# Kernel optimization log

Measured on AMD Instinct MI355X. Metric: run time of the kernel, lower is better.

Reference implementation:

```python
import jax, jax.numpy as jnp
import numpy as np

N, E, IN = 50000, 800000, 64
HC, FC1, FC2, FC3, OUT = 96, 256, 128, 64, 8
EPS = 1e-5


def setup_inputs() -> dict:
    key = jax.random.key(0)
    ks = jax.random.split(key, 24)
    def lin(k, fi, fo):
        # kaiming_uniform with relu gain: bound = sqrt(6/fi)
        b = np.sqrt(6.0 / fi)
        return jax.random.uniform(k, (fi, fo), jnp.float32, -b, b)
    inp = {
        'x': jax.random.normal(ks[0], (N, IN), jnp.float32),
        'edge_index': jax.random.randint(ks[1], (2, E), 0, N, jnp.int64),
        'w1': lin(ks[2], IN, HC), 'b1': jnp.zeros((HC,), jnp.float32),
        'g1': jax.random.uniform(ks[3], (HC,), jnp.float32, 0.5, 1.5), 'be1': jax.random.normal(ks[4], (HC,), jnp.float32) * 0.1,
        'w2': lin(ks[5], HC, HC), 'b2': jnp.zeros((HC,), jnp.float32),
        'g2': jax.random.uniform(ks[6], (HC,), jnp.float32, 0.5, 1.5), 'be2': jax.random.normal(ks[7], (HC,), jnp.float32) * 0.1,
        'w3': lin(ks[8], HC, HC), 'b3': jnp.zeros((HC,), jnp.float32),
        'g3': jax.random.uniform(ks[9], (HC,), jnp.float32, 0.5, 1.5), 'be3': jax.random.normal(ks[10], (HC,), jnp.float32) * 0.1,
        'lw1': lin(ks[11], HC, FC1), 'lb1': jnp.zeros((FC1,), jnp.float32),
        'lw2': lin(ks[12], FC1, FC2), 'lb2': jnp.zeros((FC2,), jnp.float32),
        'lw3': lin(ks[13], FC2, FC3), 'lb3': jnp.zeros((FC3,), jnp.float32),
        'lw4': lin(ks[14], FC3, OUT), 'lb4': jnp.zeros((OUT,), jnp.float32),
    }
    return inp


def _gcn(x, w, b, src, dst, norm):
    # GCNConv: out[dst] += norm_e * (x @ w)[src]; then + bias
    h = x @ w
    msg = h[src] * norm[:, None]
    return jax.ops.segment_sum(msg, dst, num_segments=N) + b


def _bn_eval(x, g, be):
    # eval-mode BatchNorm1d with running_mean=0, running_var=1
    return x / jnp.sqrt(1.0 + EPS) * g + be


def reference(x, edge_index, w1, b1, g1, be1, w2, b2, g2, be2, w3, b3, g3, be3,
              lw1, lb1, lw2, lb2, lw3, lb3, lw4, lb4):
    loops = jnp.arange(N, dtype=edge_index.dtype)
    src = jnp.concatenate([edge_index[0], loops])
    dst = jnp.concatenate([edge_index[1], loops])
    deg = jax.ops.segment_sum(jnp.ones_like(src, jnp.float32), dst, num_segments=N)
    dinv = jax.lax.rsqrt(deg)  # deg >= 1 due to self loops
    norm = dinv[src] * dinv[dst]

    h = jax.nn.relu(_bn_eval(_gcn(x, w1, b1, src, dst, norm), g1, be1))
    h = jax.nn.relu(_bn_eval(_gcn(h, w2, b2, src, dst, norm), g2, be2))
    h = jax.nn.relu(_bn_eval(_gcn(h, w3, b3, src, dst, norm), g3, be3))
    h = jax.nn.relu(h @ lw1 + lb1)
    h = jax.nn.relu(h @ lw2 + lb2)
    h = jax.nn.relu(h @ lw3 + lb3)
    return h @ lw4 + lb4
```

## Files before the change

### kernel.cpp

```cpp
#include <hip/hip_runtime.h>


#define GN 50000
#define GE 800000
#define NPART 98
#define PSLOT 9216
#define CHK 2048

typedef __attribute__((ext_vector_type(8))) short bf16x8;
typedef __attribute__((ext_vector_type(4))) float floatx4;

__device__ __forceinline__ float ar1_b2f(unsigned short h) {
    return __uint_as_float(((unsigned)h) << 16);
}
__device__ __forceinline__ unsigned short ar1_f2b(float f) {
    unsigned u = __float_as_uint(f);
    u = u + 0x7FFFu + ((u >> 16) & 1u);
    return (unsigned short)(u >> 16);
}

__global__ void ar1_detect(const int* ei, const unsigned short* xw,
                           int* flagI, int* flagF, int* gcur) {
    __shared__ int cnt;
    if (threadIdx.x == 0) cnt = 0;
    __syncthreads();
    if (blockIdx.x == 0) {
        if ((int)threadIdx.x < NPART) gcur[threadIdx.x] = 0;
        if (ei[2 * threadIdx.x + 1] != 0) atomicAdd(&cnt, 1);
        __syncthreads();
        if (threadIdx.x == 0) flagI[0] = (cnt < 8) ? 1 : 0;
    } else {
        unsigned short w = xw[2 * threadIdx.x];
        int ex = (w >> 7) & 0xFF;
        if (w == 0 || (ex >= 90 && ex <= 150)) atomicAdd(&cnt, 1);
        __syncthreads();
        if (threadIdx.x == 0) flagF[0] = (cnt > 200) ? 0 : 1;
    }
}

__global__ __launch_bounds__(256)
void ar1_part(const int* __restrict__ ei, const int* __restrict__ flagI,
              int* __restrict__ gcur, unsigned int* __restrict__ pairs, int E) {
    __shared__ int cnt[NPART], base[NPART], cur[NPART];
    int tid = (int)threadIdx.x;
    for (int i = tid; i < NPART; i += 256) { cnt[i] = 0; cur[i] = 0; }
    __syncthreads();
    int is64 = flagI[0];
    int e0 = (int)blockIdx.x * CHK;
    unsigned pk[8]; int q[8];
#pragma unroll
    for (int k = 0; k < 8; k++) {
        int e = e0 + k * 256 + tid;
        q[k] = -1; pk[k] = 0;
        if (e < E) {
            int s = is64 ? ei[2 * e] : ei[e];
            int d = is64 ? ei[2 * (E + e)] : ei[E + e];
            if ((unsigned)s < (unsigned)GN && (unsigned)d < (unsigned)GN) {
                int qq = d >> 9;
                q[k] = qq;
                pk[k] = (unsigned)s | ((unsigned)(d & 511) << 17);
                atomicAdd(&cnt[qq], 1);
            }
        }
    }
    __syncthreads();
    for (int i = tid; i < NPART; i += 256)
        base[i] = (cnt[i] > 0) ? atomicAdd(&gcur[i], cnt[i]) : 0;
    __syncthreads();
#pragma unroll
    for (int k = 0; k < 8; k++) {
        if (q[k] >= 0) {
            int r = base[q[k]] + atomicAdd(&cur[q[k]], 1);
            if (r < PSLOT) pairs[(size_t)q[k] * PSLOT + r] = pk[k];
        }
    }
}

__global__ void ar1_pscan(const int* gcur, int* pbase) {
    __shared__ int sm[128];
    int tid = (int)threadIdx.x;
    int v = (tid < NPART) ? gcur[tid] : 0;
    sm[tid] = v;
    __syncthreads();
    for (int off = 1; off < 128; off <<= 1) {
        int t = (tid >= off) ? sm[tid - off] : 0;
        __syncthreads();
        sm[tid] += t;
        __syncthreads();
    }
    if (tid < NPART) pbase[tid] = sm[tid] - v;
}

__global__ __launch_bounds__(256)
void ar1_csr(const unsigned int* __restrict__ pairs, const int* __restrict__ gcur,
             const int* __restrict__ pbase, int* __restrict__ csr,
             int* __restrict__ indeg, int* __restrict__ offs,
             float* __restrict__ dinv) {
    __shared__ int ncnt[512], pre[512], cur[512], psum[16];
    int p = (int)blockIdx.x, tid = (int)threadIdx.x;
    int cntE = gcur[p];
    if (cntE > PSLOT) cntE = PSLOT;
    int gbase = pbase[p];
    for (int i = tid; i < 512; i += 256) ncnt[i] = 0;
    __syncthreads();
    const unsigned int* pp = pairs + (size_t)p * PSLOT;
    for (int i = tid; i < cntE; i += 256) atomicAdd(&ncnt[pp[i] >> 17], 1);
    __syncthreads();
    if (tid < 16) {
        int s = 0;
        for (int j = tid * 32; j < tid * 32 + 32; j++) { pre[j] = s; s += ncnt[j]; }
        psum[tid] = s;
    }
    __syncthreads();
    if (tid == 0) {
        int s = 0;
        for (int j = 0; j < 16; j++) { int t = psum[j]; psum[j] = s; s += t; }
    }
    __syncthreads();
    if (tid < 16)
        for (int j = tid * 32; j < tid * 32 + 32; j++) pre[j] += psum[tid];
    __syncthreads();
    for (int j = tid; j < 512; j += 256) {
        cur[j] = pre[j];
        int node = p * 512 + j;
        if (node < GN) {
            indeg[node] = ncnt[j];
            offs[node] = gbase + pre[j];
            dinv[node] = rsqrtf((float)(ncnt[j] + 1));
        }
    }
    __syncthreads();
    for (int i = tid; i < cntE; i += 256) {
        unsigned v = pp[i];
        int r = atomicAdd(&cur[v >> 17], 1);
        csr[gbase + r] = (int)(v & 0x1FFFFu);
    }
}

struct SmallCvt {
    const void* src[4];
    float* dst[4];
    int n[4];
    const void* gb[9];
    float* ss[6];
};
__global__ void ar1_cvt_small(SmallCvt sc, const int* flagF) {
    int f = flagF[0];
    const float C = 0.9999950000374997f;
    for (int s = 0; s < 4; s++) {
        for (int i = threadIdx.x; i < sc.n[s]; i += 256) {
            float v = f ? ((const float*)sc.src[s])[i]
                        : ar1_b2f(((const unsigned short*)sc.src[s])[i]);
            sc.dst[s][i] = v;
        }
    }
    for (int k = 0; k < 3; k++) {
        for (int i = threadIdx.x; i < 96; i += 256) {
            float b, g, be;
            if (f) {
                b  = ((const float*)sc.gb[3 * k + 0])[i];
                g  = ((const float*)sc.gb[3 * k + 1])[i];
                be = ((const float*)sc.gb[3 * k + 2])[i];
            } else {
                b  = ar1_b2f(((const unsigned short*)sc.gb[3 * k + 0])[i]);
                g  = ar1_b2f(((const unsigned short*)sc.gb[3 * k + 1])[i]);
                be = ar1_b2f(((const unsigned short*)sc.gb[3 * k + 2])[i]);
            }
            sc.ss[2 * k + 0][i] = C * g;
            sc.ss[2 * k + 1][i] = b * C * g + be;
        }
    }
}

struct PackAll {
    const void* src[7];
    unsigned short* dst[7];
    int K[7], M[7], start[8];
};
__global__ void ar1_pack_all(PackAll pa, const int* flagF) {
    int b = (int)blockIdx.x;
    int w = 0;
    while (w < 6 && b >= pa.start[w + 1]) w++;
    int frag = b - pa.start[w];
    int K = pa.K[w], M = pa.M[w];
    int lane = (int)threadIdx.x;
    int nch = K >> 5;
    int t = frag / nch, c = frag - t * nch;
    int n = t * 16 + (lane & 15);
    int k0 = c * 32 + (lane >> 4) * 8;
    int f = flagF[0];
    unsigned short* o = pa.dst[w] + ((size_t)frag * 64 + lane) * 8;
    for (int j = 0; j < 8; j++) {
        unsigned short v = 0;
        if (n < M) {
            int idx = (k0 + j) * M + n;
            v = f ? ar1_f2b(((const float*)pa.src[w])[idx])
                  : ((const unsigned short*)pa.src[w])[idx];
        }
        o[j] = v;
    }
}

template <int NT>
__global__ __launch_bounds__(256, 2)
void ar1_mfma(const unsigned short* __restrict__ A,
              const unsigned short* __restrict__ Bp,
              const float* __restrict__ scale, const float* __restrict__ shift,
              unsigned short* __restrict__ C, int K, int Astride, int Cstride,
              int Mout) {
    int tid = (int)threadIdx.x;
    int wv = tid >> 6, lane = tid & 63;
    int mb = ((int)blockIdx.x * 4 + wv) * 16;
    int m = lane & 15, quad = lane >> 4;
    int arow = mb + m;
    if (arow >= GN) arow = GN - 1;
    const unsigned short* Aptr = A + (size_t)arow * Astride + quad * 8;
    int nch = K >> 5;

    floatx4 acc[NT];
#pragma unroll
    for (int t = 0; t < NT; t++) acc[t] = (floatx4){0.f, 0.f, 0.f, 0.f};

    for (int c = 0; c < nch; c++) {
        bf16x8 a = *((const bf16x8*)(Aptr + c * 32));
#pragma unroll
        for (int t = 0; t < NT; t++) {
            bf16x8 b = *((const bf16x8*)(Bp + ((size_t)(t * nch + c) * 64 + lane) * 8));
            acc[t] = __builtin_amdgcn_mfma_f32_16x16x32_bf16(a, b, acc[t], 0, 0, 0);
        }
    }

#pragma unroll
    for (int t = 0; t < NT; t++) {
#pragma unroll
        for (int r = 0; r < 4; r++) {
            int row = mb + quad * 4 + r;
            int col = t * 16 + m;
            if (row < GN && col < Mout) {
                float v = acc[t][r] * scale[col] + shift[col];
                C[(size_t)row * Cstride + col] = ar1_f2b(fmaxf(v, 0.f));
            }
        }
    }
}

__global__ __launch_bounds__(256, 2)
void ar1_mlp(const unsigned short* __restrict__ A,
             const unsigned short* __restrict__ b3,
             const unsigned short* __restrict__ b4,
             const unsigned short* __restrict__ b5,
             const unsigned short* __restrict__ b6,
             const float* __restrict__ lb0, const float* __restrict__ lb1,
             const float* __restrict__ lb2, const float* __restrict__ lb3,
             void* __restrict__ out, const int* __restrict__ f32out) {
    __shared__ unsigned short H1[64 * 264];
    __shared__ unsigned short H2[64 * 136];
    __shared__ unsigned short H3[64 * 72];
    int tid = (int)threadIdx.x, wv = tid >> 6, lane = tid & 63;
    int m = lane & 15, quad = lane >> 4;
    int mb = (int)blockIdx.x * 64 + wv * 16;
    int lwv = wv * 16;

    {
        int arow = mb + m; if (arow >= GN) arow = GN - 1;
        const unsigned short* Ap = A + (size_t)arow * 128 + quad * 8;
        floatx4 acc[16];
#pragma unroll
        for (int t = 0; t < 16; t++) acc[t] = (floatx4){0.f, 0.f, 0.f, 0.f};
        for (int c = 0; c < 3; c++) {
            bf16x8 a = *((const bf16x8*)(Ap + c * 32));
#pragma unroll
            for (int t = 0; t < 16; t++) {
                bf16x8 b = *((const bf16x8*)(b3 + ((size_t)(t * 3 + c) * 64 + lane) * 8));
                acc[t] = __builtin_amdgcn_mfma_f32_16x16x32_bf16(a, b, acc[t], 0, 0, 0);
            }
        }
#pragma unroll
        for (int t = 0; t < 16; t++)
#pragma unroll
            for (int r = 0; r < 4; r++) {
                int lr = lwv + quad * 4 + r, col = t * 16 + m;
                H1[lr * 264 + col] = ar1_f2b(fmaxf(acc[t][r] + lb0[col], 0.f));
            }
    }
    {
        const unsigned short* Hp = H1 + (size_t)(lwv + m) * 264 + quad * 8;
        floatx4 acc[8];
#pragma unroll
        for (int t = 0; t < 8; t++) acc[t] = (floatx4){0.f, 0.f, 0.f, 0.f};
        for (int c = 0; c < 8; c++) {
            bf16x8 a = *((const bf16x8*)(Hp + c * 32));
#pragma unroll
            for (int t = 0; t < 8; t++) {
                bf16x8 b = *((const bf16x8*)(b4 + ((size_t)(t * 8 + c) * 64 + lane) * 8));
                acc[t] = __builtin_amdgcn_mfma_f32_16x16x32_bf16(a, b, acc[t], 0, 0, 0);
            }
        }
#pragma unroll
        for (int t = 0; t < 8; t++)
#pragma unroll
            for (int r = 0; r < 4; r++) {
                int lr = lwv + quad * 4 + r, col = t * 16 + m;
                H2[lr * 136 + col] = ar1_f2b(fmaxf(acc[t][r] + lb1[col], 0.f));
            }
    }
    {
        const unsigned short* Hp = H2 + (size_t)(lwv + m) * 136 + quad * 8;
        floatx4 acc[4];
#pragma unroll
        for (int t = 0; t < 4; t++) acc[t] = (floatx4){0.f, 0.f, 0.f, 0.f};
        for (int c = 0; c < 4; c++) {
            bf16x8 a = *((const bf16x8*)(Hp + c * 32));
#pragma unroll
            for (int t = 0; t < 4; t++) {
                bf16x8 b = *((const bf16x8*)(b5 + ((size_t)(t * 4 + c) * 64 + lane) * 8));
                acc[t] = __builtin_amdgcn_mfma_f32_16x16x32_bf16(a, b, acc[t], 0, 0, 0);
            }
        }
#pragma unroll
        for (int t = 0; t < 4; t++)
#pragma unroll
            for (int r = 0; r < 4; r++) {
                int lr = lwv + quad * 4 + r, col = t * 16 + m;
                H3[lr * 72 + col] = ar1_f2b(fmaxf(acc[t][r] + lb2[col], 0.f));
            }
    }
    {
        const unsigned short* Hp = H3 + (size_t)(lwv + m) * 72 + quad * 8;
        floatx4 acc = (floatx4){0.f, 0.f, 0.f, 0.f};
        for (int c = 0; c < 2; c++) {
            bf16x8 a = *((const bf16x8*)(Hp + c * 32));
            bf16x8 b = *((const bf16x8*)(b6 + ((size_t)c * 64 + lane) * 8));
            acc = __builtin_amdgcn_mfma_f32_16x16x32_bf16(a, b, acc, 0, 0, 0);
        }
        int wf32 = f32out[0];
#pragma unroll
        for (int r = 0; r < 4; r++) {
            int row = mb + quad * 4 + r;
            if (row < GN && m < 8) {
                float v = acc[r] + lb3[m];
                if (wf32) ((float*)out)[(size_t)row * 8 + m] = v;
                else ((unsigned short*)out)[(size_t)row * 8 + m] = ar1_f2b(v);
            }
        }
    }
}

__global__ __launch_bounds__(256, 8)
void ar1_agg64(const unsigned short* __restrict__ X, const int* __restrict__ offs,
               const int* __restrict__ indeg, const int* __restrict__ csr,
               const float* __restrict__ dinv, unsigned short* __restrict__ Out) {
    int wv = (int)threadIdx.x >> 6, lane = (int)threadIdx.x & 63;
    int node = (int)blockIdx.x * 4 + wv;
    if (node >= GN) return;
    int chunk = lane & 7;
    int eslot = lane >> 3;
    float di = dinv[node];
    int off = offs[node], cnt = indeg[node];

    float acc[8];
#pragma unroll
    for (int j = 0; j < 8; j++) acc[j] = 0.f;

    for (int base = 0; base < cnt; base += 16) {
        int ss[2]; float ww[2];
#pragma unroll
        for (int k = 0; k < 2; k++) {
            int e = base + k * 8 + eslot;
            int s = node; float w = 0.f;
            if (e < cnt) {
                s = csr[off + e];
                if ((unsigned)s >= (unsigned)GN) s = node;
                w = dinv[s] * di;
            }
            ss[k] = s; ww[k] = w;
        }
        bf16x8 h0 = *((const bf16x8*)(X + (size_t)ss[0] * 64 + chunk * 8));
        bf16x8 h1 = *((const bf16x8*)(X + (size_t)ss[1] * 64 + chunk * 8));
#pragma unroll
        for (int j = 0; j < 8; j++)
            acc[j] += ww[0] * ar1_b2f((unsigned short)h0[j])
                    + ww[1] * ar1_b2f((unsigned short)h1[j]);
    }

#pragma unroll
    for (int j = 0; j < 8; j++) {
        acc[j] += __shfl_xor(acc[j], 8, 64);
        acc[j] += __shfl_xor(acc[j], 16, 64);
        acc[j] += __shfl_xor(acc[j], 32, 64);
    }

    if (eslot == 0) {
        bf16x8 hs = *((const bf16x8*)(X + (size_t)node * 64 + chunk * 8));
#pragma unroll
        for (int j = 0; j < 8; j++) {
            float v = acc[j] + di * di * ar1_b2f((unsigned short)hs[j]);
            Out[(size_t)node * 64 + chunk * 8 + j] = ar1_f2b(v);
        }
    }
}

__global__ __launch_bounds__(256, 8)
void ar1_agg96(const unsigned short* __restrict__ H, const int* __restrict__ offs,
               const int* __restrict__ indeg, const int* __restrict__ csr,
               const float* __restrict__ dinv, unsigned short* __restrict__ Out) {
    int wv = (int)threadIdx.x >> 6, lane = (int)threadIdx.x & 63;
    int node = (int)blockIdx.x * 4 + wv;
    if (node >= GN) return;
    int chunk = lane & 15;
    int eslot = lane >> 4;
    float di = dinv[node];
    int off = offs[node], cnt = indeg[node];

    float acc[8];
#pragma unroll
    for (int j = 0; j < 8; j++) acc[j] = 0.f;

    for (int base = 0; base < cnt; base += 16) {
        int ss[4]; float ww[4]; bf16x8 hh[4];
#pragma unroll
        for (int k = 0; k < 4; k++) {
            int e = base + k * 4 + eslot;
            int s = node; float w = 0.f;
            if (e < cnt) {
                s = csr[off + e];
                if ((unsigned)s >= (unsigned)GN) s = node;
                w = dinv[s] * di;
            }
            ss[k] = s; ww[k] = w;
        }
#pragma unroll
        for (int k = 0; k < 4; k++)
            hh[k] = *((const bf16x8*)(H + (size_t)ss[k] * 128 + chunk * 8));
#pragma unroll
        for (int k = 0; k < 4; k++)
#pragma unroll
            for (int j = 0; j < 8; j++)
                acc[j] += ww[k] * ar1_b2f((unsigned short)hh[k][j]);
    }

#pragma unroll
    for (int j = 0; j < 8; j++) {
        acc[j] += __shfl_xor(acc[j], 16, 64);
        acc[j] += __shfl_xor(acc[j], 32, 64);
    }

    if (eslot == 0 && chunk < 12) {
        bf16x8 hs = *((const bf16x8*)(H + (size_t)node * 128 + chunk * 8));
#pragma unroll
        for (int j = 0; j < 8; j++) {
            float v = acc[j] + di * di * ar1_b2f((unsigned short)hs[j]);
            Out[(size_t)node * 128 + chunk * 8 + j] = ar1_f2b(v);
        }
    }
}

__global__ void Arthur1_16458314678864_kernel(const void* src,
                                              unsigned short* dst, int n,
                                              const int* flagF) {
    int i = blockIdx.x * 256 + threadIdx.x;
    if (i < n) {
        if (flagF[0]) dst[i] = ar1_f2b(((const float*)src)[i]);
        else          dst[i] = ((const unsigned short*)src)[i];
    }
}

extern "C" void kernel_launch(void* const* d_in, const int* in_sizes, int n_in,
                              void* d_out, int out_size, void* d_ws, size_t ws_size,
                              hipStream_t stream) {
    (void)in_sizes; (void)n_in; (void)out_size;

    char* p = (char*)d_ws;
    unsigned short* bufA = (unsigned short*)p; p += (size_t)GN * 128 * 2;
    unsigned short* bufC = (unsigned short*)p; p += (size_t)GN * 128 * 2;
    unsigned short* bufX = (unsigned short*)p; p += (size_t)GN * 64 * 2;
    unsigned int* pairs = (unsigned int*)p; p += (size_t)NPART * PSLOT * 4;
    int* indeg  = (int*)p;    p += (size_t)GN * 4;
    int* offs   = (int*)p;    p += (size_t)GN * 4;
    float* dinv = (float*)p;  p += (size_t)GN * 4;
    int* csr    = (int*)p;    p += (size_t)GE * 4;
    int* gcur   = (int*)p;    p += 1024;
    int* pbase  = (int*)p;    p += 1024;
    int* flagI  = (int*)p;    p += 1024;
    int* flagF  = (int*)p;    p += 1024;
    unsigned short* bpArena = (unsigned short*)p; p += 91136 * 2;
    float* fArena = (float*)p; p += 2048 * 4;
    size_t need = (size_t)(p - (char*)d_ws);
    if (ws_size < need) {
        hipMemsetAsync(d_out, 0x41, (size_t)GN * 8 * 2, stream);
        return;
    }

    unsigned short* bp[7];
    int bpn[7] = {6144, 9216, 9216, 24576, 32768, 8192, 1024};
    {
        unsigned short* q = bpArena;
        for (int i = 0; i < 7; i++) { bp[i] = q; q += bpn[i]; }
    }

    float* lb[4]; float* ss[6];
    {
        float* q = fArena;
        int ln[4] = {256, 128, 64, 8};
        for (int i = 0; i < 4; i++) { lb[i] = q; q += ln[i]; }
        for (int i = 0; i < 6; i++) { ss[i] = q; q += 96; }
    }

    const int* ei = (const int*)d_in[1];

    ar1_detect<<<2, 256, 0, stream>>>(ei, (const unsigned short*)d_in[0], flagI, flagF, gcur);
    ar1_part<<<(GE + CHK - 1) / CHK, 256, 0, stream>>>(ei, flagI, gcur, pairs, GE);
    ar1_pscan<<<1, 128, 0, stream>>>(gcur, pbase);
    ar1_csr<<<NPART, 256, 0, stream>>>(pairs, gcur, pbase, csr, indeg, offs, dinv);

    Arthur1_16458314678864_kernel<<<(GN * 64 + 255) / 256, 256, 0, stream>>>(
        d_in[0], bufX, GN * 64, flagF);
    {
        SmallCvt sc;
        int lsrc[4] = {15, 17, 19, 21};
        int ln[4] = {256, 128, 64, 8};
        for (int i = 0; i < 4; i++) { sc.src[i] = d_in[lsrc[i]]; sc.dst[i] = lb[i]; sc.n[i] = ln[i]; }
        int gsrc[9] = {3, 4, 5, 7, 8, 9, 11, 12, 13};
        for (int i = 0; i < 9; i++) sc.gb[i] = d_in[gsrc[i]];
        for (int i = 0; i < 6; i++) sc.ss[i] = ss[i];
        ar1_cvt_small<<<1, 256, 0, stream>>>(sc, flagF);
    }
    {
        PackAll pa;
        int wsrc[7] = {2, 6, 10, 14, 16, 18, 20};
        int Ks[7] = {64, 96, 96, 96, 256, 128, 64};
        int Ms[7] = {96, 96, 96, 256, 128, 64, 8};
        int cum = 0;
        for (int i = 0; i < 7; i++) {
            pa.src[i] = d_in[wsrc[i]]; pa.dst[i] = bp[i];
            pa.K[i] = Ks[i]; pa.M[i] = Ms[i];
            pa.start[i] = cum;
            cum += (Ms[i] + 15) / 16 * (Ks[i] / 32);
        }
        pa.start[7] = cum;
        ar1_pack_all<<<cum, 64, 0, stream>>>(pa, flagF);
    }

    const int GB = (GN + 63) / 64;
    const int AB = GN / 4;

    ar1_agg64<<<AB, 256, 0, stream>>>(bufX, offs, indeg, csr, dinv, bufC);
    ar1_mfma<6><<<GB, 256, 0, stream>>>(bufC, bp[0], ss[0], ss[1], bufA, 64, 64, 128, 96);
    ar1_agg96<<<AB, 256, 0, stream>>>(bufA, offs, indeg, csr, dinv, bufC);
    ar1_mfma<6><<<GB, 256, 0, stream>>>(bufC, bp[1], ss[2], ss[3], bufA, 96, 128, 128, 96);
    ar1_agg96<<<AB, 256, 0, stream>>>(bufA, offs, indeg, csr, dinv, bufC);
    ar1_mfma<6><<<GB, 256, 0, stream>>>(bufC, bp[2], ss[4], ss[5], bufA, 96, 128, 128, 96);

    ar1_mlp<<<GB, 256, 0, stream>>>(bufA, bp[3], bp[4], bp[5], bp[6],
                                    lb[0], lb[1], lb[2], lb[3], d_out, flagF);
}
```

Before: 331.5 us.

## Pack hidden buffers to 96-wide rows, read input directly, merge setup kernels

Hidden activation buffers shrink from a 128-element row stride to 96, so the gathers in aggregation and the matmul stores move less padding, and agg96 is re-laned to use 48 of 64 lanes with 12 chunks. The separate kernel that converted x to bf16 is removed; agg64 now reads the raw input in fp32 or bf16 depending on a flag. The small-parameter conversion and weight-packing kernels are fused into one launch to cut launch overhead. The cost is a quarter of the lanes idle in agg96, shuffle-based reductions in place of xor butterflies, and fp32 gathers of x in the first layer.

Result: faster. 324.7 us (-2.0%).

```diff
diff --git a/kernel.cpp b/kernel.cpp
--- a/kernel.cpp
+++ b/kernel.cpp
@@ -137,6 +137,11 @@
     }
 }
 
+struct PackAll {
+    const void* src[7];
+    unsigned short* dst[7];
+    int K[7], M[7], start[8];
+};
 struct SmallCvt {
     const void* src[4];
     float* dst[4];
@@ -144,60 +149,58 @@
     const void* gb[9];
     float* ss[6];
 };
-__global__ void ar1_cvt_small(SmallCvt sc, const int* flagF) {
+
+__global__ void Arthur1_16458314678864_kernel(PackAll pa, SmallCvt sc,
+                                              const int* flagF) {
+    int b = (int)blockIdx.x;
     int f = flagF[0];
-    const float C = 0.9999950000374997f;
-    for (int s = 0; s < 4; s++) {
-        for (int i = threadIdx.x; i < sc.n[s]; i += 256) {
-            float v = f ? ((const float*)sc.src[s])[i]
-                        : ar1_b2f(((const unsigned short*)sc.src[s])[i]);
-            sc.dst[s][i] = v;
-        }
-    }
-    for (int k = 0; k < 3; k++) {
-        for (int i = threadIdx.x; i < 96; i += 256) {
-            float b, g, be;
-            if (f) {
-                b  = ((const float*)sc.gb[3 * k + 0])[i];
-                g  = ((const float*)sc.gb[3 * k + 1])[i];
-                be = ((const float*)sc.gb[3 * k + 2])[i];
-            } else {
-                b  = ar1_b2f(((const unsigned short*)sc.gb[3 * k + 0])[i]);
-                g  = ar1_b2f(((const unsigned short*)sc.gb[3 * k + 1])[i]);
-                be = ar1_b2f(((const unsigned short*)sc.gb[3 * k + 2])[i]);
-            }
-            sc.ss[2 * k + 0][i] = C * g;
-            sc.ss[2 * k + 1][i] = b * C * g + be;
-        }
-    }
-}
-
-struct PackAll {
-    const void* src[7];
-    unsigned short* dst[7];
-    int K[7], M[7], start[8];
-};
-__global__ void ar1_pack_all(PackAll pa, const int* flagF) {
-    int b = (int)blockIdx.x;
-    int w = 0;
-    while (w < 6 && b >= pa.start[w + 1]) w++;
-    int frag = b - pa.start[w];
-    int K = pa.K[w], M = pa.M[w];
-    int lane = (int)threadIdx.x;
-    int nch = K >> 5;
-    int t = frag / nch, c = frag - t * nch;
-    int n = t * 16 + (lane & 15);
-    int k0 = c * 32 + (lane >> 4) * 8;
-    int f = flagF[0];
-    unsigned short* o = pa.dst[w] + ((size_t)frag * 64 + lane) * 8;
-    for (int j = 0; j < 8; j++) {
-        unsigned short v = 0;
-        if (n < M) {
-            int idx = (k0 + j) * M + n;
-            v = f ? ar1_f2b(((const float*)pa.src[w])[idx])
-                  : ((const unsigned short*)pa.src[w])[idx];
-        }
-        o[j] = v;
+    if (b < 45) {
+        int frag_g = b * 4 + ((int)threadIdx.x >> 6);
+        if (frag_g >= 178) return;
+        int w = 0;
+        while (w < 6 && frag_g >= pa.start[w + 1]) w++;
+        int frag = frag_g - pa.start[w];
+        int K = pa.K[w], M = pa.M[w];
+        int lane = (int)threadIdx.x & 63;
+        int nch = K >> 5;
+        int t = frag / nch, c = frag - t * nch;
+        int n = t * 16 + (lane & 15);
+        int k0 = c * 32 + (lane >> 4) * 8;
+        unsigned short* o = pa.dst[w] + ((size_t)frag * 64 + lane) * 8;
+        for (int j = 0; j < 8; j++) {
+            unsigned short v = 0;
+            if (n < M) {
+                int idx = (k0 + j) * M + n;
+                v = f ? ar1_f2b(((const float*)pa.src[w])[idx])
+                      : ((const unsigned short*)pa.src[w])[idx];
+            }
+            o[j] = v;
+        }
+    } else {
+        const float C = 0.9999950000374997f;
+        for (int s = 0; s < 4; s++) {
+            for (int i = threadIdx.x; i < sc.n[s]; i += 256) {
+                float v = f ? ((const float*)sc.src[s])[i]
+                            : ar1_b2f(((const unsigned short*)sc.src[s])[i]);
+                sc.dst[s][i] = v;
+            }
+        }
+        for (int k = 0; k < 3; k++) {
+            for (int i = threadIdx.x; i < 96; i += 256) {
+                float bb, g, be;
+                if (f) {
+                    bb = ((const float*)sc.gb[3 * k + 0])[i];
+                    g  = ((const float*)sc.gb[3 * k + 1])[i];
+                    be = ((const float*)sc.gb[3 * k + 2])[i];
+                } else {
+                    bb = ar1_b2f(((const unsigned short*)sc.gb[3 * k + 0])[i]);
+                    g  = ar1_b2f(((const unsigned short*)sc.gb[3 * k + 1])[i]);
+                    be = ar1_b2f(((const unsigned short*)sc.gb[3 * k + 2])[i]);
+                }
+                sc.ss[2 * k + 0][i] = C * g;
+                sc.ss[2 * k + 1][i] = bb * C * g + be;
+            }
+        }
     }
 }
 
@@ -206,8 +209,7 @@
 void ar1_mfma(const unsigned short* __restrict__ A,
               const unsigned short* __restrict__ Bp,
               const float* __restrict__ scale, const float* __restrict__ shift,
-              unsigned short* __restrict__ C, int K, int Astride, int Cstride,
-              int Mout) {
+              unsigned short* __restrict__ C, int K, int Astride, int Cstride) {
     int tid = (int)threadIdx.x;
     int wv = tid >> 6, lane = tid & 63;
     int mb = ((int)blockIdx.x * 4 + wv) * 16;
@@ -236,7 +238,7 @@
         for (int r = 0; r < 4; r++) {
             int row = mb + quad * 4 + r;
             int col = t * 16 + m;
-            if (row < GN && col < Mout) {
+            if (row < GN) {
                 float v = acc[t][r] * scale[col] + shift[col];
                 C[(size_t)row * Cstride + col] = ar1_f2b(fmaxf(v, 0.f));
             }
@@ -263,7 +265,7 @@
 
     {
         int arow = mb + m; if (arow >= GN) arow = GN - 1;
-        const unsigned short* Ap = A + (size_t)arow * 128 + quad * 8;
+        const unsigned short* Ap = A + (size_t)arow * 96 + quad * 8;
         floatx4 acc[16];
 #pragma unroll
         for (int t = 0; t < 16; t++) acc[t] = (floatx4){0.f, 0.f, 0.f, 0.f};
@@ -347,9 +349,10 @@
 }
 
 __global__ __launch_bounds__(256, 8)
-void ar1_agg64(const unsigned short* __restrict__ X, const int* __restrict__ offs,
+void ar1_agg64(const void* __restrict__ Xv, const int* __restrict__ offs,
                const int* __restrict__ indeg, const int* __restrict__ csr,
-               const float* __restrict__ dinv, unsigned short* __restrict__ Out) {
+               const float* __restrict__ dinv, const int* __restrict__ flagF,
+               unsigned short* __restrict__ Out) {
     int wv = (int)threadIdx.x >> 6, lane = (int)threadIdx.x & 63;
     int node = (int)blockIdx.x * 4 + wv;
     if (node >= GN) return;
@@ -357,6 +360,9 @@
     int eslot = lane >> 3;
     float di = dinv[node];
     int off = offs[node], cnt = indeg[node];
+    int f = flagF[0];
+    const unsigned short* X16 = (const unsigned short*)Xv;
+    const float* X32 = (const float*)Xv;
 
     float acc[8];
 #pragma unroll
@@ -375,12 +381,22 @@
             }
             ss[k] = s; ww[k] = w;
         }
-        bf16x8 h0 = *((const bf16x8*)(X + (size_t)ss[0] * 64 + chunk * 8));
-        bf16x8 h1 = *((const bf16x8*)(X + (size_t)ss[1] * 64 + chunk * 8));
-#pragma unroll
-        for (int j = 0; j < 8; j++)
-            acc[j] += ww[0] * ar1_b2f((unsigned short)h0[j])
-                    + ww[1] * ar1_b2f((unsigned short)h1[j]);
+#pragma unroll
+        for (int k = 0; k < 2; k++) {
+            float hv[8];
+            if (f) {
+                floatx4 a = *((const floatx4*)(X32 + (size_t)ss[k] * 64 + chunk * 8));
+                floatx4 b = *((const floatx4*)(X32 + (size_t)ss[k] * 64 + chunk * 8 + 4));
+#pragma unroll
+                for (int j = 0; j < 4; j++) { hv[j] = a[j]; hv[4 + j] = b[j]; }
+            } else {
+                bf16x8 h = *((const bf16x8*)(X16 + (size_t)ss[k] * 64 + chunk * 8));
+#pragma unroll
+                for (int j = 0; j < 8; j++) hv[j] = ar1_b2f((unsigned short)h[j]);
+            }
+#pragma unroll
+            for (int j = 0; j < 8; j++) acc[j] += ww[k] * hv[j];
+        }
     }
 
 #pragma unroll
@@ -391,10 +407,20 @@
     }
 
     if (eslot == 0) {
-        bf16x8 hs = *((const bf16x8*)(X + (size_t)node * 64 + chunk * 8));
+        float hv[8];
+        if (f) {
+            floatx4 a = *((const floatx4*)(X32 + (size_t)node * 64 + chunk * 8));
+            floatx4 b = *((const floatx4*)(X32 + (size_t)node * 64 + chunk * 8 + 4));
+#pragma unroll
+            for (int j = 0; j < 4; j++) { hv[j] = a[j]; hv[4 + j] = b[j]; }
+        } else {
+            bf16x8 h = *((const bf16x8*)(X16 + (size_t)node * 64 + chunk * 8));
+#pragma unroll
+            for (int j = 0; j < 8; j++) hv[j] = ar1_b2f((unsigned short)h[j]);
+        }
 #pragma unroll
         for (int j = 0; j < 8; j++) {
-            float v = acc[j] + di * di * ar1_b2f((unsigned short)hs[j]);
+            float v = acc[j] + di * di * hv[j];
             Out[(size_t)node * 64 + chunk * 8 + j] = ar1_f2b(v);
         }
     }
@@ -407,8 +433,9 @@
     int wv = (int)threadIdx.x >> 6, lane = (int)threadIdx.x & 63;
     int node = (int)blockIdx.x * 4 + wv;
     if (node >= GN) return;
-    int chunk = lane & 15;
-    int eslot = lane >> 4;
+    int chunk = lane % 12;
+    int eslot = lane / 12;
+    int active = (lane < 48) ? 1 : 0;
     float di = dinv[node];
     int off = offs[node], cnt = indeg[node];
 
@@ -416,52 +443,46 @@
 #pragma unroll
     for (int j = 0; j < 8; j++) acc[j] = 0.f;
 
-    for (int base = 0; base < cnt; base += 16) {
-        int ss[4]; float ww[4]; bf16x8 hh[4];
-#pragma unroll
-        for (int k = 0; k < 4; k++) {
-            int e = base + k * 4 + eslot;
-            int s = node; float w = 0.f;
-            if (e < cnt) {
-                s = csr[off + e];
-                if ((unsigned)s >= (unsigned)GN) s = node;
-                w = dinv[s] * di;
-            }
-            ss[k] = s; ww[k] = w;
-        }
-#pragma unroll
-        for (int k = 0; k < 4; k++)
-            hh[k] = *((const bf16x8*)(H + (size_t)ss[k] * 128 + chunk * 8));
-#pragma unroll
-        for (int k = 0; k < 4; k++)
-#pragma unroll
-            for (int j = 0; j < 8; j++)
-                acc[j] += ww[k] * ar1_b2f((unsigned short)hh[k][j]);
+    if (active) {
+        for (int base = 0; base < cnt; base += 16) {
+            int ss[4]; float ww[4]; bf16x8 hh[4];
+#pragma unroll
+            for (int k = 0; k < 4; k++) {
+                int e = base + k * 4 + eslot;
+                int s = node; float w = 0.f;
+                if (e < cnt) {
+                    s = csr[off + e];
+                    if ((unsigned)s >= (unsigned)GN) s = node;
+                    w = dinv[s] * di;
+                }
+                ss[k] = s; ww[k] = w;
+            }
+#pragma unroll
+            for (int k = 0; k < 4; k++)
+                hh[k] = *((const bf16x8*)(H + (size_t)ss[k] * 96 + chunk * 8));
+#pragma unroll
+            for (int k = 0; k < 4; k++)
+#pragma unroll
+                for (int j = 0; j < 8; j++)
+                    acc[j] += ww[k] * ar1_b2f((unsigned short)hh[k][j]);
+        }
     }
 
 #pragma unroll
     for (int j = 0; j < 8; j++) {
-        acc[j] += __shfl_xor(acc[j], 16, 64);
-        acc[j] += __shfl_xor(acc[j], 32, 64);
-    }
-
-    if (eslot == 0 && chunk < 12) {
-        bf16x8 hs = *((const bf16x8*)(H + (size_t)node * 128 + chunk * 8));
+        float a1 = __shfl(acc[j], lane + 12, 64);
+        float a2 = __shfl(acc[j], lane + 24, 64);
+        float a3 = __shfl(acc[j], lane + 36, 64);
+        acc[j] += a1 + a2 + a3;
+    }
+
+    if (lane < 12) {
+        bf16x8 hs = *((const bf16x8*)(H + (size_t)node * 96 + chunk * 8));
 #pragma unroll
         for (int j = 0; j < 8; j++) {
             float v = acc[j] + di * di * ar1_b2f((unsigned short)hs[j]);
-            Out[(size_t)node * 128 + chunk * 8 + j] = ar1_f2b(v);
-        }
-    }
-}
-
-__global__ void Arthur1_16458314678864_kernel(const void* src,
-                                              unsigned short* dst, int n,
-                                              const int* flagF) {
-    int i = blockIdx.x * 256 + threadIdx.x;
-    if (i < n) {
-        if (flagF[0]) dst[i] = ar1_f2b(((const float*)src)[i]);
-        else          dst[i] = ((const unsigned short*)src)[i];
+            Out[(size_t)node * 96 + chunk * 8 + j] = ar1_f2b(v);
+        }
     }
 }
 
@@ -471,9 +492,8 @@
     (void)in_sizes; (void)n_in; (void)out_size;
 
     char* p = (char*)d_ws;
-    unsigned short* bufA = (unsigned short*)p; p += (size_t)GN * 128 * 2;
-    unsigned short* bufC = (unsigned short*)p; p += (size_t)GN * 128 * 2;
-    unsigned short* bufX = (unsigned short*)p; p += (size_t)GN * 64 * 2;
+    unsigned short* bufA = (unsigned short*)p; p += (size_t)GN * 96 * 2;
+    unsigned short* bufC = (unsigned short*)p; p += (size_t)GN * 96 * 2;
     unsigned int* pairs = (unsigned int*)p; p += (size_t)NPART * PSLOT * 4;
     int* indeg  = (int*)p;    p += (size_t)GN * 4;
     int* offs   = (int*)p;    p += (size_t)GN * 4;
@@ -513,18 +533,6 @@
     ar1_pscan<<<1, 128, 0, stream>>>(gcur, pbase);
     ar1_csr<<<NPART, 256, 0, stream>>>(pairs, gcur, pbase, csr, indeg, offs, dinv);
 
-    Arthur1_16458314678864_kernel<<<(GN * 64 + 255) / 256, 256, 0, stream>>>(
-        d_in[0], bufX, GN * 64, flagF);
-    {
-        SmallCvt sc;
-        int lsrc[4] = {15, 17, 19, 21};
-        int ln[4] = {256, 128, 64, 8};
-        for (int i = 0; i < 4; i++) { sc.src[i] = d_in[lsrc[i]]; sc.dst[i] = lb[i]; sc.n[i] = ln[i]; }
-        int gsrc[9] = {3, 4, 5, 7, 8, 9, 11, 12, 13};
-        for (int i = 0; i < 9; i++) sc.gb[i] = d_in[gsrc[i]];
-        for (int i = 0; i < 6; i++) sc.ss[i] = ss[i];
-        ar1_cvt_small<<<1, 256, 0, stream>>>(sc, flagF);
-    }
     {
         PackAll pa;
         int wsrc[7] = {2, 6, 10, 14, 16, 18, 20};
@@ -538,18 +546,25 @@
             cum += (Ms[i] + 15) / 16 * (Ks[i] / 32);
         }
         pa.start[7] = cum;
-        ar1_pack_all<<<cum, 64, 0, stream>>>(pa, flagF);
+        SmallCvt sc;
+        int lsrc[4] = {15, 17, 19, 21};
+        int ln[4] = {256, 128, 64, 8};
+        for (int i = 0; i < 4; i++) { sc.src[i] = d_in[lsrc[i]]; sc.dst[i] = lb[i]; sc.n[i] = ln[i]; }
+        int gsrc[9] = {3, 4, 5, 7, 8, 9, 11, 12, 13};
+        for (int i = 0; i < 9; i++) sc.gb[i] = d_in[gsrc[i]];
+        for (int i = 0; i < 6; i++) sc.ss[i] = ss[i];
+        Arthur1_16458314678864_kernel<<<46, 256, 0, stream>>>(pa, sc, flagF);
     }
 
     const int GB = (GN + 63) / 64;
     const int AB = GN / 4;
 
-    ar1_agg64<<<AB, 256, 0, stream>>>(bufX, offs, indeg, csr, dinv, bufC);
-    ar1_mfma<6><<<GB, 256, 0, stream>>>(bufC, bp[0], ss[0], ss[1], bufA, 64, 64, 128, 96);
+    ar1_agg64<<<AB, 256, 0, stream>>>(d_in[0], offs, indeg, csr, dinv, flagF, bufC);
+    ar1_mfma<6><<<GB, 256, 0, stream>>>(bufC, bp[0], ss[0], ss[1], bufA, 64, 64, 96);
     ar1_agg96<<<AB, 256, 0, stream>>>(bufA, offs, indeg, csr, dinv, bufC);
-    ar1_mfma<6><<<GB, 256, 0, stream>>>(bufC, bp[1], ss[2], ss[3], bufA, 96, 128, 128, 96);
+    ar1_mfma<6><<<GB, 256, 0, stream>>>(bufC, bp[1], ss[2], ss[3], bufA, 96, 96, 96);
     ar1_agg96<<<AB, 256, 0, stream>>>(bufA, offs, indeg, csr, dinv, bufC);
-    ar1_mfma<6><<<GB, 256, 0, stream>>>(bufC, bp[2], ss[4], ss[5], bufA, 96, 128, 128, 96);
+    ar1_mfma<6><<<GB, 256, 0, stream>>>(bufC, bp[2], ss[4], ss[5], bufA, 96, 96, 96);
 
     ar1_mlp<<<GB, 256, 0, stream>>>(bufA, bp[3], bp[4], bp[5], bp[6],
                                     lb[0], lb[1], lb[2], lb[3], d_out, flagF);
```
